# Optimization experiments

Hardware: AMD Instinct MI355X
Metric: run time of the kernel (lower is better)

Reference implementation:

```python
import jax, jax.numpy as jnp
import numpy as np
import math

# ----- sizes -----
NUM_EDGES = 16384
NUM_NODES = 1024          # senders index into [0, NUM_NODES)
N_MUL = 64                # multiplicity n = V.shape[1]
AVG_NEIGH = 16.0          # avg_num_neighbors
F_IN = 64                 # scalar feature dim of x

# ----- real spherical harmonics (component normalization: sum_m Y_lm^2 = 2l+1) -----
_S3 = math.sqrt(3.0); _S5 = math.sqrt(5.0); _S15 = math.sqrt(15.0)
_C33 = math.sqrt(70.0)/4.0; _C32 = math.sqrt(105.0)/2.0
_C31 = math.sqrt(42.0)/4.0; _C30 = math.sqrt(7.0)/2.0; _CXYZ = math.sqrt(105.0)

def _sph(vn):
    x, y, z = vn[:, 0], vn[:, 1], vn[:, 2]
    Y0 = jnp.ones_like(x)[:, None]
    Y1 = _S3 * vn
    Y2 = jnp.stack([_S15*x*y, _S15*y*z, 0.5*_S5*(3*z*z - 1), _S15*x*z, 0.5*_S15*(x*x - y*y)], axis=1)
    Y3 = jnp.stack([_C33*y*(3*x*x - y*y), _CXYZ*x*y*z, _C31*y*(5*z*z - 1), _C30*z*(5*z*z - 3), _C31*x*(5*z*z - 1), _C32*z*(x*x - y*y), _C33*x*(x*x - 3*y*y)], axis=1)
    return [Y0, Y1, Y2, Y3]

# monomial form of the same SH, used to derive EXACT Clebsch-Gordan coefficients
_SHP = {
    0: [[(1.0, (0,0,0))]],
    1: [[(_S3, (1,0,0))], [(_S3, (0,1,0))], [(_S3, (0,0,1))]],
    2: [[(_S15, (1,1,0))], [(_S15, (0,1,1))], [(1.5*_S5, (0,0,2)), (-0.5*_S5, (0,0,0))], [(_S15, (1,0,1))], [(0.5*_S15, (2,0,0)), (-0.5*_S15, (0,2,0))]],
    3: [[(3*_C33, (2,1,0)), (-_C33, (0,3,0))], [(_CXYZ, (1,1,1))], [(5*_C31, (0,1,2)), (-_C31, (0,1,0))], [(5*_C30, (0,0,3)), (-3*_C30, (0,0,1))], [(5*_C31, (1,0,2)), (-_C31, (1,0,0))], [(_C32, (2,0,1)), (-_C32, (0,2,1))], [(_C33, (3,0,0)), (-3*_C33, (1,2,0))]],
}

def _dfact(n):
    r = 1
    while n > 1:
        r *= n; n -= 2
    return r

def _mono_int(e):
    # exact integral of x^a y^b z^c over the unit sphere
    a, b, c = e
    if (a % 2) or (b % 2) or (c % 2):
        return 0.0
    return 4.0*math.pi*_dfact(a-1)*_dfact(b-1)*_dfact(c-1)/_dfact(a+b+c+1)

def _pmul(p, q):
    return [(cp*cq, (a1+a2, b1+b2, c1+c2)) for cp, (a1,b1,c1) in p for cq, (a2,b2,c2) in q]

def _pint(p):
    return sum(c*_mono_int(e) for c, e in p)

def _cg(l1, l2, l3):
    # unique SO(3) intertwiner in this real-SH basis, scaled like e3nn component norm: sqrt(2l3+1)*w3j
    C = np.zeros((2*l1+1, 2*l2+1, 2*l3+1))
    for i, p1 in enumerate(_SHP[l1]):
        for j, p2 in enumerate(_SHP[l2]):
            p12 = _pmul(p1, p2)
            for k, p3 in enumerate(_SHP[l3]):
                C[i, j, k] = _pint(_pmul(p12, p3)) / (4.0*math.pi)
    return jnp.asarray(C / np.linalg.norm(C) * np.sqrt(2*l3+1), dtype=jnp.float32)

# tensor-product paths surviving filter_ir_out = 0e + 1o + 2e (inputs: SH 0e+1o+2e+3o, V 0e+1o+2e)
_PATHS0 = [(0,0), (1,1), (2,2)]
_PATHS1 = [(0,1), (1,0), (1,2), (2,1), (3,2)]
_PATHS2 = [(0,2), (1,1), (2,0), (2,2), (3,1)]
CGS = {(l1, l2, l3): _cg(l1, l2, l3) for l3, ps in ((0, _PATHS0), (1, _PATHS1), (2, _PATHS2)) for l1, l2 in ps}

# e3nn normalize_function(silu): divide by sqrt(E_{z~N(0,1)}[silu(z)^2])
_zg = np.linspace(-12.0, 12.0, 200001)
_phi = np.exp(-0.5*_zg*_zg)/np.sqrt(2.0*np.pi)
_sl = _zg/(1.0 + np.exp(-_zg))
ACT_C = float(np.sqrt(np.sum(_sl*_sl*_phi)*(_zg[1]-_zg[0])))

def _nsilu(v):
    return jax.nn.silu(v) / ACT_C

def _forward(vectors, x, V, senders, W_w, W1, W2, W3, Wv1, Wv2):
    E, n = V.shape[0], V.shape[1]
    d = jnp.linalg.norm(vectors, axis=1, keepdims=True)                 # [E,1] edge lengths
    vn = vectors / d
    Y = jnp.concatenate(_sph(vn), axis=1)                               # [E,16], ell = 0..3
    w = (x @ W_w) / math.sqrt(x.shape[1])                               # [E,n] edge weights (1-layer MLP, no act)
    wY = w[:, :, None] * Y[:, None, :]                                  # [E,n,16]
    agg = jax.ops.segment_sum(wY, senders, num_segments=NUM_NODES)[senders]  # scatter_sum + map_back
    agg = agg / math.sqrt(AVG_NEIGH)
    A = jnp.split(agg, [1, 4, 9], axis=2)                               # SH chunks: dims 1,3,5,7
    B = jnp.split(V, [1, 4], axis=2)                                    # V chunks: dims 1,3,5
    def tp(l1, l2, l3):
        return jnp.einsum('eni,enj,ijk->enk', A[l1], B[l2], CGS[(l1, l2, l3)])
    scal = jnp.concatenate([tp(a, b, 0) for a, b in _PATHS0], axis=2)   # [E,n,3] new scalars
    V1 = jnp.concatenate([tp(a, b, 1) for a, b in _PATHS1], axis=1)     # [E,5n,3] 1o paths
    V2 = jnp.concatenate([tp(a, b, 2) for a, b in _PATHS2], axis=1)     # [E,5n,5] 2e paths
    h = jnp.concatenate([x, scal.reshape(E, 3*n)], axis=1)              # [E, F_IN+3n]
    h = _nsilu(h @ W1 / math.sqrt(h.shape[1]))
    h = _nsilu(h @ W2 / math.sqrt(W2.shape[0]))
    h = h @ W3 / math.sqrt(W3.shape[0])                                 # output_activation=False
    # poly_envelope(p-1=5, 2), p=6: 1 - 28 d^6 + 48 d^7 - 21 d^8 on [0,1), 0 outside
    u = 1.0 - 28.0*d**6 + 48.0*d**7 - 21.0*d**8
    x_out = jnp.where(d < 1.0, u, 0.0) * h                              # [E,64]
    o1 = jnp.einsum('emi,mo->eoi', V1, Wv1) / math.sqrt(V1.shape[1])    # Linear per irrep: [E,n,3]
    o2 = jnp.einsum('emi,mo->eoi', V2, Wv2) / math.sqrt(V2.shape[1])    # [E,n,5]
    # output 0e block has no input path -> zeros (e3nn Linear, no bias)
    V_out = jnp.concatenate([jnp.zeros((E, n, 1), x_out.dtype), o1, o2], axis=2)  # [E,n,9]
    return x_out, V_out

def setup_inputs():
    key = jax.random.key(0)
    ks = jax.random.split(key, 10)
    E = NUM_EDGES
    vectors = 0.35 * jax.random.normal(ks[0], (E, 3), jnp.float32)   # mostly inside cutoff radius 1
    x = jax.random.normal(ks[1], (E, F_IN), jnp.float32)
    V = jax.random.normal(ks[2], (E, N_MUL, 9), jnp.float32)
    senders = jax.random.randint(ks[3], (E,), 0, NUM_NODES, dtype=jnp.int32)
    W_w = jax.random.normal(ks[4], (F_IN, N_MUL), jnp.float32)
    W1 = jax.random.normal(ks[5], (F_IN + 3*N_MUL, 64), jnp.float32)
    W2 = jax.random.normal(ks[6], (64, 64), jnp.float32)
    W3 = jax.random.normal(ks[7], (64, 64), jnp.float32)
    Wv1 = jax.random.normal(ks[8], (5*N_MUL, N_MUL), jnp.float32)
    Wv2 = jax.random.normal(ks[9], (5*N_MUL, N_MUL), jnp.float32)
    return {"vectors": vectors, "x": x, "V": V, "senders": senders, "W_w": W_w, "W1": W1, "W2": W2, "W3": W3, "Wv1": Wv1, "Wv2": Wv2}

def reference(vectors, x, V, senders, W_w, W1, W2, W3, Wv1, Wv2):
    return _forward(vectors, x, V, senders, W_w, W1, W2, W3, Wv1, Wv2)
```

## Files before the change

### kernel.cpp

```cpp
#include <hip/hip_runtime.h>
#include <math.h>

#define NNODES 1024
#define EB 8

typedef __attribute__((ext_vector_type(8))) short short8;
typedef __attribute__((ext_vector_type(4))) float f32x4;

__device__ __forceinline__ unsigned short f2bf(float f) {
  union { float f; unsigned int u; } v; v.f = f;
  unsigned int r = v.u + 0x7fffu + ((v.u >> 16) & 1u);
  return (unsigned short)(r >> 16);
}

struct CGPack { float v[576]; };

static const double H_SHC[16][2] = {
  {1.0, 0.0},
  {1.7320508075688772, 0.0},
  {1.7320508075688772, 0.0},
  {1.7320508075688772, 0.0},
  {3.8729833462074170, 0.0},
  {3.8729833462074170, 0.0},
  {3.3541019662496844, -1.1180339887498949},
  {3.8729833462074170, 0.0},
  {1.9364916731037085, -1.9364916731037085},
  {6.2749501990055667, -2.0916500663351889},
  {10.246950765959598, 0.0},
  {8.1009258730098255, -1.6201851746019651},
  {6.6143782776614768, -3.9686269665968861},
  {8.1009258730098255, -1.6201851746019651},
  {5.1234753829797990, -5.1234753829797990},
  {2.0916500663351889, -6.2749501990055667},
};
static const int H_SHE[16][2] = {
  {0,0},{1,0},{16,0},{256,0},
  {17,0},{272,0},{512,0},{257,0},{2,32},
  {18,48},{273,0},{528,16},{768,256},{513,1},{258,288},{3,33}};
static const int H_PL1[13] = {0,1,2, 0,1,1,2,3, 0,1,2,2,3};
static const int H_PL2[13] = {0,1,2, 1,0,2,1,2, 2,1,0,2,1};
static const int H_PL3[13] = {0,0,0, 1,1,1,1,1, 2,2,2,2,2};
static const int H_PCG[13] = {0,1,10, 35,44,53,98,143, 248,273,318,343,468};

static double h_dfact(int n) { double r = 1.0; while (n > 1) { r *= n; n -= 2; } return r; }

struct HostConsts {
  CGPack pack;
  float inv_actc;
  HostConsts() {
    const int LOFF[4] = {0,1,4,9};
    for (int p = 0; p < 13; p++) {
      int l1 = H_PL1[p], l2 = H_PL2[p], l3 = H_PL3[p];
      int n1 = 2*l1+1, n2 = 2*l2+1, n3 = 2*l3+1, nent = n1*n2*n3;
      double vals[125], ss = 0.0;
      for (int t = 0; t < nent; t++) {
        int i = t / (n2*n3);
        int rem = t - i*(n2*n3);
        int j = rem / n3;
        int k = rem - j*n3;
        int lm1 = LOFF[l1]+i, lm2 = LOFF[l2]+j, lm3 = LOFF[l3]+k;
        double v = 0.0;
        for (int t1 = 0; t1 < 2; t1++)
        for (int t2 = 0; t2 < 2; t2++)
        for (int t3 = 0; t3 < 2; t3++) {
          double cc = H_SHC[lm1][t1]*H_SHC[lm2][t2]*H_SHC[lm3][t3];
          if (cc == 0.0) continue;
          int s = H_SHE[lm1][t1] + H_SHE[lm2][t2] + H_SHE[lm3][t3];
          int a = s & 15, b = (s >> 4) & 15, c = (s >> 8) & 15;
          if (!((a|b|c) & 1))
            v += cc * (h_dfact(a-1)*h_dfact(b-1)*h_dfact(c-1) / h_dfact(a+b+c+1));
        }
        vals[t] = v; ss += v*v;
      }
      double scale = sqrt((double)(2*l3+1)) / sqrt(ss);
      for (int t = 0; t < nent; t++) pack.v[H_PCG[p]+t] = (float)(vals[t]*scale*0.25);
    }
    pack.v[573] = pack.v[574] = pack.v[575] = 0.f;
    double s = 0.0, dz = 24.0/200000.0;
    for (int i = 0; i <= 200000; i++) {
      double z = -12.0 + dz*i;
      double ph = exp(-0.5*z*z) * 0.39894228040143267794;
      double sl = z / (1.0 + exp(-z));
      s += sl*sl*ph;
    }
    inv_actc = (float)(1.0 / sqrt(s*dz));
  }
};

__global__ __launch_bounds__(256) void k_pre(
    const int* __restrict__ senders, int* __restrict__ counts, int* __restrict__ elist,
    const float* __restrict__ Wv1, const float* __restrict__ Wv2,
    const float* __restrict__ W1, const float* __restrict__ W2, const float* __restrict__ W3,
    unsigned short* __restrict__ wv1f, unsigned short* __restrict__ wv2f,
    unsigned short* __restrict__ w1f, unsigned short* __restrict__ w2f,
    unsigned short* __restrict__ w3f,
    float inv_actc, int E)
{
  const int t = threadIdx.x;
  const int nsc = gridDim.x - 32;
  if ((int)blockIdx.x < nsc) {
    int e = blockIdx.x*256 + t;
    if (e < E) {
      int s = senders[e];
      int pos = atomicAdd(&counts[s], 1) & 63;
      elist[s*64 + pos] = e;
    }
    return;
  }
  const int wid = t >> 6, lane = t & 63;
  const int g = (blockIdx.x - nsc)*4 + wid;
  const float ia = inv_actc;
  const float s320 = 0.05590169943749474f;
  const float* src; unsigned short* dst; int nk, f; float sc;
  if (g < 40)       { src = Wv1; dst = wv1f; nk = 10; f = g;       sc = s320; }
  else if (g < 80)  { src = Wv2; dst = wv2f; nk = 10; f = g - 40;  sc = s320; }
  else if (g < 112) { src = W1;  dst = w1f;  nk = 8;  f = g - 80;  sc = 0.0625f; }
  else if (g < 120) { src = W2;  dst = w2f;  nk = 2;  f = g - 112; sc = 0.125f*ia; }
  else              { src = W3;  dst = w3f;  nk = 2;  f = g - 120; sc = 0.125f*ia; }
  int nt = f / nk;
  int ks = f - nt*nk;
  unsigned short us[8];
  #pragma unroll
  for (int j = 0; j < 8; j++) {
    float v = src[(ks*32 + (lane>>4)*8 + j)*64 + nt*16 + (lane & 15)];
    us[j] = f2bf(v * sc);
  }
  uint4 pk;
  pk.x = (unsigned)us[0] | ((unsigned)us[1] << 16);
  pk.y = (unsigned)us[2] | ((unsigned)us[3] << 16);
  pk.z = (unsigned)us[4] | ((unsigned)us[5] << 16);
  pk.w = (unsigned)us[6] | ((unsigned)us[7] << 16);
  *(uint4*)(dst + ((size_t)f*64 + lane)*8) = pk;
}

__global__ __launch_bounds__(256, 2) void k_node(
    const float* __restrict__ vec, const float* __restrict__ x,
    const float* __restrict__ Ww,
    const int* __restrict__ counts, const int* __restrict__ elist,
    float* __restrict__ node_agg)
{
  __shared__ float red[4*1024];
  const int wid = threadIdx.x >> 6, lane = threadIdx.x & 63;
  const int s = blockIdx.x;
  const int deg = min(counts[s], 64);

  float ww[64];
  #pragma unroll
  for (int f = 0; f < 64; f++) ww[f] = Ww[f*64 + lane];

  const float S3 = 1.7320508075688772f, S5 = 2.23606797749979f, S15 = 3.872983346207417f;
  const float C33 = 2.091650066335189f, C32 = 5.123475382979799f, C31 = 1.6201851746019651f;
  const float C30 = 1.3228756555322954f, CX = 10.246950765959598f;

  float A[16];
  #pragma unroll
  for (int k = 0; k < 16; k++) A[k] = 0.f;

  for (int ii = wid; ii < deg; ii += 4) {
    int e = elist[s*64 + ii];
    float xv = x[(size_t)e*64 + lane];
    float w0 = 0.f, w1 = 0.f, w2 = 0.f, w3 = 0.f;
    #pragma unroll
    for (int f = 0; f < 64; f += 4) {
      w0 = fmaf(__shfl(xv, f+0), ww[f+0], w0);
      w1 = fmaf(__shfl(xv, f+1), ww[f+1], w1);
      w2 = fmaf(__shfl(xv, f+2), ww[f+2], w2);
      w3 = fmaf(__shfl(xv, f+3), ww[f+3], w3);
    }
    float w = ((w0+w1)+(w2+w3)) * 0.125f;
    float vx = vec[e*3+0], vy = vec[e*3+1], vz = vec[e*3+2];
    float d = sqrtf(vx*vx + vy*vy + vz*vz);
    float X = vx/d, Yv = vy/d, Z = vz/d;
    float y[16];
    y[0] = 1.f;
    y[1] = S3*X;  y[2] = S3*Yv;  y[3] = S3*Z;
    y[4] = S15*X*Yv; y[5] = S15*Yv*Z; y[6] = 0.5f*S5*(3.f*Z*Z - 1.f);
    y[7] = S15*X*Z;  y[8] = 0.5f*S15*(X*X - Yv*Yv);
    y[9]  = C33*Yv*(3.f*X*X - Yv*Yv);
    y[10] = CX*X*Yv*Z;
    y[11] = C31*Yv*(5.f*Z*Z - 1.f);
    y[12] = C30*Z*(5.f*Z*Z - 3.f);
    y[13] = C31*X*(5.f*Z*Z - 1.f);
    y[14] = C32*Z*(X*X - Yv*Yv);
    y[15] = C33*X*(X*X - 3.f*Yv*Yv);
    #pragma unroll
    for (int k = 0; k < 16; k++) A[k] = fmaf(w, y[k], A[k]);
  }
  #pragma unroll
  for (int k = 0; k < 16; k++) red[wid*1024 + lane*16 + k] = A[k];
  __syncthreads();
  const int t = threadIdx.x;
  f32x4 v0 = ((f32x4*)red)[t];
  f32x4 v1 = ((f32x4*)red)[256 + t];
  f32x4 v2 = ((f32x4*)red)[512 + t];
  f32x4 v3 = ((f32x4*)red)[768 + t];
  f32x4 sum = v0 + v1 + v2 + v3;
  ((f32x4*)(node_agg + (size_t)s*1024))[t] = sum;
}

template<int L1, int L2, int L3>
__device__ __forceinline__ void tp_path(const float* __restrict__ cgp,
    const float a[16], const float b[9], float o[2*L3+1])
{
  constexpr int N1 = 2*L1+1, N2 = 2*L2+1, N3 = 2*L3+1;
  constexpr int AO = (L1==0) ? 0 : (L1==1) ? 1 : (L1==2) ? 4 : 9;
  constexpr int BO = (L2==0) ? 0 : (L2==1) ? 1 : 4;
  constexpr int LM1 = (L1==0) ? 0 : (L1==1) ? 1 : (L1==2) ? 4 : 9;
  constexpr int LM2 = (L2==0) ? 0 : (L2==1) ? 1 : 4;
  constexpr int LM3 = (L3==0) ? 0 : (L3==1) ? 1 : 4;
  static constexpr unsigned char PAR[16] =
      {0, 1,2,4, 3,6,0,5,0, 2,7,2,4,1,4,1};
  #pragma unroll
  for (int k = 0; k < N3; k++) o[k] = 0.f;
  int ci = 0;
  #pragma unroll
  for (int i = 0; i < N1; i++) {
    #pragma unroll
    for (int j = 0; j < N2; j++) {
      float ab = a[AO+i] * b[BO+j];
      #pragma unroll
      for (int k = 0; k < N3; k++) {
        if ((PAR[LM1+i] ^ PAR[LM2+j] ^ PAR[LM3+k]) == 0)
          o[k] = fmaf(ab, cgp[ci], o[k]);
        ci++;
      }
    }
  }
}

__global__ __launch_bounds__(256, 3) void edge_main(
    const float* __restrict__ vec, const float* __restrict__ x,
    const float* __restrict__ V, const int* __restrict__ senders,
    const float* __restrict__ node_agg, const CGPack P,
    const unsigned short* __restrict__ wv1f, const unsigned short* __restrict__ wv2f,
    const unsigned short* __restrict__ w1f, const unsigned short* __restrict__ w2f,
    const unsigned short* __restrict__ w3f,
    float* __restrict__ out, int E)
{
  __shared__ __align__(16) unsigned short V12sh[64*328];
  __shared__ __align__(16) unsigned short zrow[336];
  __shared__ __align__(16) unsigned short hsh[8*264];
  __shared__ __align__(16) unsigned short h1sh[8*72];
  __shared__ __align__(16) unsigned short h2sh[8*72];
  __shared__ __align__(16) float xosh[8*64];
  __shared__ float ush[EB];

  unsigned short* V1sh = V12sh;
  unsigned short* V2sh = V12sh + 24*328;
  float* vosh = (float*)V12sh;

  const float* cg = P.v;

  const int t = threadIdx.x;
  const int wid = t >> 6, lane = t & 63;
  const int e0 = blockIdx.x * EB;
  const size_t E64 = (size_t)E * 64;

  if (t < 168) ((unsigned int*)zrow)[t] = 0u;

  if (t < 128) {
    int el = t >> 4, off = (t & 15)*4;
    f32x4 xv = *(const f32x4*)(x + (size_t)(e0 + el)*64 + off);
    uint2 pk;
    pk.x = (unsigned)f2bf(xv.x) | ((unsigned)f2bf(xv.y) << 16);
    pk.y = (unsigned)f2bf(xv.z) | ((unsigned)f2bf(xv.w) << 16);
    *(uint2*)(hsh + el*264 + off) = pk;
  }

  #pragma unroll
  for (int sub = 0; sub < 2; sub++) {
    const int eloc = wid*2 + sub;
    const int eg = e0 + eloc;

    float b[9];
    const float* vp = V + (size_t)eg*576 + lane*9;
    #pragma unroll
    for (int j = 0; j < 9; j++) b[j] = vp[j];

    const int s = senders[eg];
    float a[16];
    const float* nap = node_agg + s*1024 + lane*16;
    #pragma unroll
    for (int k = 0; k < 16; k++) a[k] = nap[k];

    float o1[1], o3[3], o5[5];
    tp_path<0,0,0>(cg + 0,  a, b, o1); hsh[eloc*264 + 64 + lane*3 + 0] = f2bf(o1[0]);
    tp_path<1,1,0>(cg + 1,  a, b, o1); hsh[eloc*264 + 64 + lane*3 + 1] = f2bf(o1[0]);
    tp_path<2,2,0>(cg + 10, a, b, o1); hsh[eloc*264 + 64 + lane*3 + 2] = f2bf(o1[0]);
    tp_path<0,1,1>(cg + 35, a, b, o3);
    { int r = eloc*3; for (int i=0;i<3;i++) V1sh[(r+i)*328 + 0*64 + lane] = f2bf(o3[i]); }
    tp_path<1,0,1>(cg + 44, a, b, o3);
    { int r = eloc*3; for (int i=0;i<3;i++) V1sh[(r+i)*328 + 1*64 + lane] = f2bf(o3[i]); }
    tp_path<1,2,1>(cg + 53, a, b, o3);
    { int r = eloc*3; for (int i=0;i<3;i++) V1sh[(r+i)*328 + 2*64 + lane] = f2bf(o3[i]); }
    tp_path<2,1,1>(cg + 98, a, b, o3);
    { int r = eloc*3; for (int i=0;i<3;i++) V1sh[(r+i)*328 + 3*64 + lane] = f2bf(o3[i]); }
    tp_path<3,2,1>(cg + 143, a, b, o3);
    { int r = eloc*3; for (int i=0;i<3;i++) V1sh[(r+i)*328 + 4*64 + lane] = f2bf(o3[i]); }
    tp_path<0,2,2>(cg + 248, a, b, o5);
    { int r = eloc*5; for (int i=0;i<5;i++) V2sh[(r+i)*328 + 0*64 + lane] = f2bf(o5[i]); }
    tp_path<1,1,2>(cg + 273, a, b, o5);
    { int r = eloc*5; for (int i=0;i<5;i++) V2sh[(r+i)*328 + 1*64 + lane] = f2bf(o5[i]); }
    tp_path<2,0,2>(cg + 318, a, b, o5);
    { int r = eloc*5; for (int i=0;i<5;i++) V2sh[(r+i)*328 + 2*64 + lane] = f2bf(o5[i]); }
    tp_path<2,2,2>(cg + 343, a, b, o5);
    { int r = eloc*5; for (int i=0;i<5;i++) V2sh[(r+i)*328 + 3*64 + lane] = f2bf(o5[i]); }
    tp_path<3,1,2>(cg + 468, a, b, o5);
    { int r = eloc*5; for (int i=0;i<5;i++) V2sh[(r+i)*328 + 4*64 + lane] = f2bf(o5[i]); }

    if (lane == 0) {
      float vx = vec[eg*3+0], vy = vec[eg*3+1], vz = vec[eg*3+2];
      float d = sqrtf(vx*vx + vy*vy + vz*vz);
      float u = 0.f;
      if (d < 1.f) {
        float d3 = d*d*d, d6 = d3*d3, d7 = d6*d, d8 = d7*d;
        u = 1.f - 28.f*d6 + 48.f*d7 - 21.f*d8;
      }
      ush[eloc] = u;
    }
  }
  __syncthreads();

  const int ntile = wid;
  const int qr = lane >> 4;
  const int ml = lane & 15;

  f32x4 acc1a = (f32x4){0,0,0,0}, acc1b = (f32x4){0,0,0,0};
  {
    const unsigned short* p0 = &V1sh[ml*328];
    const unsigned short* p1 = (16+ml < 24) ? &V1sh[(16+ml)*328] : zrow;
    const unsigned short* bb = wv1f + ((size_t)(ntile*10)*64 + lane)*8;
    #pragma unroll
    for (int ks = 0; ks < 10; ks++) {
      short8 bf = *(const short8*)(bb + ks*512);
      int ao = ks*32 + qr*8;
      short8 af0 = *(const short8*)(p0 + ao);
      short8 af1 = *(const short8*)(p1 + ao);
      acc1a = __builtin_amdgcn_mfma_f32_16x16x32_bf16(af0, bf, acc1a, 0, 0, 0);
      acc1b = __builtin_amdgcn_mfma_f32_16x16x32_bf16(af1, bf, acc1b, 0, 0, 0);
    }
  }

  f32x4 acc2a = (f32x4){0,0,0,0}, acc2b = (f32x4){0,0,0,0}, acc2c = (f32x4){0,0,0,0};
  {
    const unsigned short* p0 = &V2sh[ml*328];
    const unsigned short* p1 = &V2sh[(16+ml)*328];
    const unsigned short* p2 = (32+ml < 40) ? &V2sh[(32+ml)*328] : zrow;
    const unsigned short* bb = wv2f + ((size_t)(ntile*10)*64 + lane)*8;
    #pragma unroll
    for (int ks = 0; ks < 10; ks++) {
      short8 bf = *(const short8*)(bb + ks*512);
      int ao = ks*32 + qr*8;
      short8 af0 = *(const short8*)(p0 + ao);
      short8 af1 = *(const short8*)(p1 + ao);
      short8 af2 = *(const short8*)(p2 + ao);
      acc2a = __builtin_amdgcn_mfma_f32_16x16x32_bf16(af0, bf, acc2a, 0, 0, 0);
      acc2b = __builtin_amdgcn_mfma_f32_16x16x32_bf16(af1, bf, acc2b, 0, 0, 0);
      acc2c = __builtin_amdgcn_mfma_f32_16x16x32_bf16(af2, bf, acc2c, 0, 0, 0);
    }
  }

  {
    f32x4 c = (f32x4){0,0,0,0};
    const unsigned short* hp = (ml < 8) ? &hsh[ml*264] : zrow;
    const unsigned short* bb = w1f + ((size_t)(ntile*8)*64 + lane)*8;
    #pragma unroll
    for (int ks = 0; ks < 8; ks++) {
      short8 bf = *(const short8*)(bb + ks*512);
      short8 af = *(const short8*)(hp + ks*32 + qr*8);
      c = __builtin_amdgcn_mfma_f32_16x16x32_bf16(af, bf, c, 0, 0, 0);
    }
    #pragma unroll
    for (int r = 0; r < 4; r++) {
      int row = qr*4 + r;
      if (row < 8) {
        float v = c[r];
        float sv = v / (1.f + expf(-v));
        h1sh[row*72 + ntile*16 + ml] = f2bf(sv);
      }
    }
  }
  __syncthreads();

  #pragma unroll
  for (int r = 0; r < 4; r++) {
    int row = qr*4 + r;
    int el = row / 3, i = row - (row/3)*3;
    vosh[el*584 + (ntile*16+ml)*9 + 1 + i] = acc1a[r];
  }
  #pragma unroll
  for (int r = 0; r < 4; r++) {
    int row = 16 + qr*4 + r;
    if (row < 24) {
      int el = row / 3, i = row - (row/3)*3;
      vosh[el*584 + (ntile*16+ml)*9 + 1 + i] = acc1b[r];
    }
  }
  #pragma unroll
  for (int r = 0; r < 4; r++) {
    int row = qr*4 + r;
    int el = row / 5, i = row - (row/5)*5;
    vosh[el*584 + (ntile*16+ml)*9 + 4 + i] = acc2a[r];
  }
  #pragma unroll
  for (int r = 0; r < 4; r++) {
    int row = 16 + qr*4 + r;
    int el = row / 5, i = row - (row/5)*5;
    vosh[el*584 + (ntile*16+ml)*9 + 4 + i] = acc2b[r];
  }
  #pragma unroll
  for (int r = 0; r < 4; r++) {
    int row = 32 + qr*4 + r;
    if (row < 40) {
      int el = row / 5, i = row - (row/5)*5;
      vosh[el*584 + (ntile*16+ml)*9 + 4 + i] = acc2c[r];
    }
  }
  for (int q = t; q < 8*64; q += 256) {
    int el = q >> 6, n = q & 63;
    vosh[el*584 + n*9] = 0.f;
  }

  {
    f32x4 c = (f32x4){0,0,0,0};
    const unsigned short* ap = (ml < 8) ? &h1sh[ml*72] : zrow;
    const unsigned short* bb = w2f + ((size_t)(ntile*2)*64 + lane)*8;
    #pragma unroll
    for (int ks = 0; ks < 2; ks++) {
      short8 bf = *(const short8*)(bb + ks*512);
      short8 af = *(const short8*)(ap + ks*32 + qr*8);
      c = __builtin_amdgcn_mfma_f32_16x16x32_bf16(af, bf, c, 0, 0, 0);
    }
    #pragma unroll
    for (int r = 0; r < 4; r++) {
      int row = qr*4 + r;
      if (row < 8) {
        float v = c[r];
        float sv = v / (1.f + expf(-v));
        h2sh[row*72 + ntile*16 + ml] = f2bf(sv);
      }
    }
  }
  __syncthreads();

  {
    f32x4 c = (f32x4){0,0,0,0};
    const unsigned short* ap = (ml < 8) ? &h2sh[ml*72] : zrow;
    const unsigned short* bb = w3f + ((size_t)(ntile*2)*64 + lane)*8;
    #pragma unroll
    for (int ks = 0; ks < 2; ks++) {
      short8 bf = *(const short8*)(bb + ks*512);
      short8 af = *(const short8*)(ap + ks*32 + qr*8);
      c = __builtin_amdgcn_mfma_f32_16x16x32_bf16(af, bf, c, 0, 0, 0);
    }
    #pragma unroll
    for (int r = 0; r < 4; r++) {
      int row = qr*4 + r;
      if (row < 8) xosh[row*64 + ntile*16 + ml] = ush[row] * c[r];
    }
  }

  for (int q = t; q < 8*144; q += 256) {
    int el = q / 144, i4 = q - (q/144)*144;
    ((f32x4*)(out + E64 + (size_t)(e0+el)*576))[i4] = ((f32x4*)(vosh + el*584))[i4];
  }
  __syncthreads();

  if (t < 128)
    ((f32x4*)(out + (size_t)e0*64))[t] = ((f32x4*)xosh)[t];
}

extern "C" void kernel_launch(void* const* d_in, const int* in_sizes, int n_in,
                              void* d_out, int out_size, void* d_ws, size_t ws_size,
                              hipStream_t stream)
{
  const float* vec     = (const float*)d_in[0];
  const float* x       = (const float*)d_in[1];
  const float* V       = (const float*)d_in[2];
  const int*   senders = (const int*)  d_in[3];
  const float* Ww      = (const float*)d_in[4];
  const float* W1      = (const float*)d_in[5];
  const float* W2      = (const float*)d_in[6];
  const float* W3      = (const float*)d_in[7];
  const float* Wv1     = (const float*)d_in[8];
  const float* Wv2     = (const float*)d_in[9];
  float* out = (float*)d_out;
  const int E = in_sizes[0] / 3;

  static HostConsts HC;

  char* base = (char*)d_ws;
  float* node_agg = (float*)(base);
  int* counts     = (int*)  (base + (8<<20) + 8192);
  int* elist      = (int*)  (base + (8<<20) + 12288);
  unsigned short* wv1f = (unsigned short*)(base + (8<<20) + 278528);
  unsigned short* wv2f = (unsigned short*)(base + (8<<20) + 319488);
  unsigned short* w1f  = (unsigned short*)(base + (8<<20) + 360448);
  unsigned short* w2f  = (unsigned short*)(base + (8<<20) + 393216);
  unsigned short* w3f  = (unsigned short*)(base + (8<<20) + 401408);

  hipMemsetAsync(counts, 0, NNODES*sizeof(int), stream);

  const int nsc = (E + 255) >> 8;
  k_pre<<<nsc + 32, 256, 0, stream>>>(senders, counts, elist,
                                      Wv1, Wv2, W1, W2, W3,
                                      wv1f, wv2f, w1f, w2f, w3f, HC.inv_actc, E);
  k_node<<<NNODES, 256, 0, stream>>>(vec, x, Ww, counts, elist, node_agg);
  edge_main<<<E/EB, 256, 0, stream>>>(vec, x, V, senders, node_agg, HC.pack,
                                      wv1f, wv2f, w1f, w2f, w3f, out, E);
}
```

Before: 171.8 us.

## Precompute edge weights in k_pre and halve edges per block in edge_main

Moves the per-edge x·W_w product out of k_node's gather loop into extra k_pre blocks that tile 64 edges in shared memory and write the result to a workspace buffer. k_node then only loads the precomputed weight instead of running a shuffle-based matvec for every neighbour. edge_main now handles 4 edges per block, one per wave, instead of 8. Its shared-memory footprint shrinks and the launch bound rises to 6 blocks per CU to raise occupancy, at the cost of more padded MFMA rows and twice as many blocks. A redundant dead y[14] assignment is also added.

New measurement: 165.9 us. 1.04x faster.

```diff
diff --git a/kernel.cpp b/kernel.cpp
--- a/kernel.cpp
+++ b/kernel.cpp
@@ -2,7 +2,7 @@
 #include <math.h>
 
 #define NNODES 1024
-#define EB 8
+#define EB 4
 
 typedef __attribute__((ext_vector_type(8))) short short8;
 typedef __attribute__((ext_vector_type(4))) float f32x4;
@@ -89,6 +89,8 @@
 
 __global__ __launch_bounds__(256) void k_pre(
     const int* __restrict__ senders, int* __restrict__ counts, int* __restrict__ elist,
+    const float* __restrict__ x, const float* __restrict__ Ww,
+    float* __restrict__ w_ws,
     const float* __restrict__ Wv1, const float* __restrict__ Wv2,
     const float* __restrict__ W1, const float* __restrict__ W2, const float* __restrict__ W3,
     unsigned short* __restrict__ wv1f, unsigned short* __restrict__ wv2f,
@@ -97,9 +99,11 @@
     float inv_actc, int E)
 {
   const int t = threadIdx.x;
-  const int nsc = gridDim.x - 32;
-  if ((int)blockIdx.x < nsc) {
-    int e = blockIdx.x*256 + t;
+  const int bid = blockIdx.x;
+  const int nsc = (E + 255) >> 8;
+
+  if (bid < nsc) {
+    int e = bid*256 + t;
     if (e < E) {
       int s = senders[e];
       int pos = atomicAdd(&counts[s], 1) & 63;
@@ -107,35 +111,66 @@
     }
     return;
   }
-  const int wid = t >> 6, lane = t & 63;
-  const int g = (blockIdx.x - nsc)*4 + wid;
-  const float ia = inv_actc;
-  const float s320 = 0.05590169943749474f;
-  const float* src; unsigned short* dst; int nk, f; float sc;
-  if (g < 40)       { src = Wv1; dst = wv1f; nk = 10; f = g;       sc = s320; }
-  else if (g < 80)  { src = Wv2; dst = wv2f; nk = 10; f = g - 40;  sc = s320; }
-  else if (g < 112) { src = W1;  dst = w1f;  nk = 8;  f = g - 80;  sc = 0.0625f; }
-  else if (g < 120) { src = W2;  dst = w2f;  nk = 2;  f = g - 112; sc = 0.125f*ia; }
-  else              { src = W3;  dst = w3f;  nk = 2;  f = g - 120; sc = 0.125f*ia; }
-  int nt = f / nk;
-  int ks = f - nt*nk;
-  unsigned short us[8];
-  #pragma unroll
-  for (int j = 0; j < 8; j++) {
-    float v = src[(ks*32 + (lane>>4)*8 + j)*64 + nt*16 + (lane & 15)];
-    us[j] = f2bf(v * sc);
-  }
-  uint4 pk;
-  pk.x = (unsigned)us[0] | ((unsigned)us[1] << 16);
-  pk.y = (unsigned)us[2] | ((unsigned)us[3] << 16);
-  pk.z = (unsigned)us[4] | ((unsigned)us[5] << 16);
-  pk.w = (unsigned)us[6] | ((unsigned)us[7] << 16);
-  *(uint4*)(dst + ((size_t)f*64 + lane)*8) = pk;
+
+  if (bid < nsc + 32) {
+    const int wid = t >> 6, lane = t & 63;
+    const int g = (bid - nsc)*4 + wid;
+    const float ia = inv_actc;
+    const float s320 = 0.05590169943749474f;
+    const float* src; unsigned short* dst; int nk, f; float sc;
+    if (g < 40)       { src = Wv1; dst = wv1f; nk = 10; f = g;       sc = s320; }
+    else if (g < 80)  { src = Wv2; dst = wv2f; nk = 10; f = g - 40;  sc = s320; }
+    else if (g < 112) { src = W1;  dst = w1f;  nk = 8;  f = g - 80;  sc = 0.0625f; }
+    else if (g < 120) { src = W2;  dst = w2f;  nk = 2;  f = g - 112; sc = 0.125f*ia; }
+    else              { src = W3;  dst = w3f;  nk = 2;  f = g - 120; sc = 0.125f*ia; }
+    int nt = f / nk;
+    int ks = f - nt*nk;
+    unsigned short us[8];
+    #pragma unroll
+    for (int j = 0; j < 8; j++) {
+      float v = src[(ks*32 + (lane>>4)*8 + j)*64 + nt*16 + (lane & 15)];
+      us[j] = f2bf(v * sc);
+    }
+    uint4 pk;
+    pk.x = (unsigned)us[0] | ((unsigned)us[1] << 16);
+    pk.y = (unsigned)us[2] | ((unsigned)us[3] << 16);
+    pk.z = (unsigned)us[4] | ((unsigned)us[5] << 16);
+    pk.w = (unsigned)us[6] | ((unsigned)us[7] << 16);
+    *(uint4*)(dst + ((size_t)f*64 + lane)*8) = pk;
+    return;
+  }
+
+  __shared__ float xsh[64*64];
+  const int eb0 = (bid - nsc - 32) * 64;
+  for (int q = t; q < 1024; q += 256)
+    ((f32x4*)xsh)[q] = ((const f32x4*)(x + (size_t)eb0*64))[q];
+
+  const int n = t & 63;
+  float ww[64];
+  #pragma unroll
+  for (int f = 0; f < 64; f++) ww[f] = Ww[f*64 + n];
+  __syncthreads();
+
+  const int er0 = (t >> 6) * 16;
+  #pragma unroll
+  for (int i = 0; i < 16; i++) {
+    int e = er0 + i;
+    const f32x4* xr = (const f32x4*)(&xsh[e*64]);
+    float a0 = 0.f, a1 = 0.f, a2 = 0.f, a3 = 0.f;
+    #pragma unroll
+    for (int fq = 0; fq < 16; fq += 4) {
+      f32x4 x0 = xr[fq+0], x1 = xr[fq+1], x2 = xr[fq+2], x3 = xr[fq+3];
+      a0 = fmaf(x0.x, ww[fq*4+0],  fmaf(x0.y, ww[fq*4+1],  fmaf(x0.z, ww[fq*4+2],  fmaf(x0.w, ww[fq*4+3],  a0))));
+      a1 = fmaf(x1.x, ww[fq*4+4],  fmaf(x1.y, ww[fq*4+5],  fmaf(x1.z, ww[fq*4+6],  fmaf(x1.w, ww[fq*4+7],  a1))));
+      a2 = fmaf(x2.x, ww[fq*4+8],  fmaf(x2.y, ww[fq*4+9],  fmaf(x2.z, ww[fq*4+10], fmaf(x2.w, ww[fq*4+11], a2))));
+      a3 = fmaf(x3.x, ww[fq*4+12], fmaf(x3.y, ww[fq*4+13], fmaf(x3.z, ww[fq*4+14], fmaf(x3.w, ww[fq*4+15], a3))));
+    }
+    w_ws[(size_t)(eb0+e)*64 + n] = ((a0+a1)+(a2+a3)) * 0.125f;
+  }
 }
 
-__global__ __launch_bounds__(256, 2) void k_node(
-    const float* __restrict__ vec, const float* __restrict__ x,
-    const float* __restrict__ Ww,
+__global__ __launch_bounds__(256) void k_node(
+    const float* __restrict__ vec, const float* __restrict__ w_ws,
     const int* __restrict__ counts, const int* __restrict__ elist,
     float* __restrict__ node_agg)
 {
@@ -144,10 +179,6 @@
   const int s = blockIdx.x;
   const int deg = min(counts[s], 64);
 
-  float ww[64];
-  #pragma unroll
-  for (int f = 0; f < 64; f++) ww[f] = Ww[f*64 + lane];
-
   const float S3 = 1.7320508075688772f, S5 = 2.23606797749979f, S15 = 3.872983346207417f;
   const float C33 = 2.091650066335189f, C32 = 5.123475382979799f, C31 = 1.6201851746019651f;
   const float C30 = 1.3228756555322954f, CX = 10.246950765959598f;
@@ -158,16 +189,7 @@
 
   for (int ii = wid; ii < deg; ii += 4) {
     int e = elist[s*64 + ii];
-    float xv = x[(size_t)e*64 + lane];
-    float w0 = 0.f, w1 = 0.f, w2 = 0.f, w3 = 0.f;
-    #pragma unroll
-    for (int f = 0; f < 64; f += 4) {
-      w0 = fmaf(__shfl(xv, f+0), ww[f+0], w0);
-      w1 = fmaf(__shfl(xv, f+1), ww[f+1], w1);
-      w2 = fmaf(__shfl(xv, f+2), ww[f+2], w2);
-      w3 = fmaf(__shfl(xv, f+3), ww[f+3], w3);
-    }
-    float w = ((w0+w1)+(w2+w3)) * 0.125f;
+    float wv = w_ws[(size_t)e*64 + lane];
     float vx = vec[e*3+0], vy = vec[e*3+1], vz = vec[e*3+2];
     float d = sqrtf(vx*vx + vy*vy + vz*vz);
     float X = vx/d, Yv = vy/d, Z = vz/d;
@@ -181,10 +203,11 @@
     y[11] = C31*Yv*(5.f*Z*Z - 1.f);
     y[12] = C30*Z*(5.f*Z*Z - 3.f);
     y[13] = C31*X*(5.f*Z*Z - 1.f);
+    y[14] = C32*Z*(X*X - 3.f*Yv*Yv)*0.f + C32*Z*(X*X - Yv*Yv);
     y[14] = C32*Z*(X*X - Yv*Yv);
     y[15] = C33*X*(X*X - 3.f*Yv*Yv);
     #pragma unroll
-    for (int k = 0; k < 16; k++) A[k] = fmaf(w, y[k], A[k]);
+    for (int k = 0; k < 16; k++) A[k] = fmaf(wv, y[k], A[k]);
   }
   #pragma unroll
   for (int k = 0; k < 16; k++) red[wid*1024 + lane*16 + k] = A[k];
@@ -228,7 +251,7 @@
   }
 }
 
-__global__ __launch_bounds__(256, 3) void edge_main(
+__global__ __launch_bounds__(256, 6) void edge_main(
     const float* __restrict__ vec, const float* __restrict__ x,
     const float* __restrict__ V, const int* __restrict__ senders,
     const float* __restrict__ node_agg, const CGPack P,
@@ -237,16 +260,16 @@
     const unsigned short* __restrict__ w3f,
     float* __restrict__ out, int E)
 {
-  __shared__ __align__(16) unsigned short V12sh[64*328];
+  __shared__ __align__(16) unsigned short V12sh[32*328];
   __shared__ __align__(16) unsigned short zrow[336];
-  __shared__ __align__(16) unsigned short hsh[8*264];
-  __shared__ __align__(16) unsigned short h1sh[8*72];
-  __shared__ __align__(16) unsigned short h2sh[8*72];
-  __shared__ __align__(16) float xosh[8*64];
+  __shared__ __align__(16) unsigned short hsh[4*264];
+  __shared__ __align__(16) unsigned short h1sh[4*72];
+  __shared__ __align__(16) unsigned short h2sh[4*72];
+  __shared__ __align__(16) float xosh[4*64];
   __shared__ float ush[EB];
 
   unsigned short* V1sh = V12sh;
-  unsigned short* V2sh = V12sh + 24*328;
+  unsigned short* V2sh = V12sh + 12*328;
   float* vosh = (float*)V12sh;
 
   const float* cg = P.v;
@@ -258,7 +281,7 @@
 
   if (t < 168) ((unsigned int*)zrow)[t] = 0u;
 
-  if (t < 128) {
+  if (t < 64) {
     int el = t >> 4, off = (t & 15)*4;
     f32x4 xv = *(const f32x4*)(x + (size_t)(e0 + el)*64 + off);
     uint2 pk;
@@ -267,9 +290,8 @@
     *(uint2*)(hsh + el*264 + off) = pk;
   }
 
-  #pragma unroll
-  for (int sub = 0; sub < 2; sub++) {
-    const int eloc = wid*2 + sub;
+  {
+    const int eloc = wid;
     const int eg = e0 + eloc;
 
     float b[9];
@@ -279,9 +301,12 @@
 
     const int s = senders[eg];
     float a[16];
-    const float* nap = node_agg + s*1024 + lane*16;
-    #pragma unroll
-    for (int k = 0; k < 16; k++) a[k] = nap[k];
+    const f32x4* nap = (const f32x4*)(node_agg + s*1024 + lane*16);
+    #pragma unroll
+    for (int q = 0; q < 4; q++) {
+      f32x4 av = nap[q];
+      a[q*4+0] = av.x; a[q*4+1] = av.y; a[q*4+2] = av.z; a[q*4+3] = av.w;
+    }
 
     float o1[1], o3[3], o5[5];
     tp_path<0,0,0>(cg + 0,  a, b, o1); hsh[eloc*264 + 64 + lane*3 + 0] = f2bf(o1[0]);
@@ -325,44 +350,37 @@
   const int qr = lane >> 4;
   const int ml = lane & 15;
 
-  f32x4 acc1a = (f32x4){0,0,0,0}, acc1b = (f32x4){0,0,0,0};
+  f32x4 acc1 = (f32x4){0,0,0,0};
   {
-    const unsigned short* p0 = &V1sh[ml*328];
-    const unsigned short* p1 = (16+ml < 24) ? &V1sh[(16+ml)*328] : zrow;
+    const unsigned short* p0 = (ml < 12) ? &V1sh[ml*328] : zrow;
     const unsigned short* bb = wv1f + ((size_t)(ntile*10)*64 + lane)*8;
+    #pragma unroll
+    for (int ks = 0; ks < 10; ks++) {
+      short8 bf = *(const short8*)(bb + ks*512);
+      short8 af = *(const short8*)(p0 + ks*32 + qr*8);
+      acc1 = __builtin_amdgcn_mfma_f32_16x16x32_bf16(af, bf, acc1, 0, 0, 0);
+    }
+  }
+
+  f32x4 acc2a = (f32x4){0,0,0,0}, acc2b = (f32x4){0,0,0,0};
+  {
+    const unsigned short* p0 = &V2sh[ml*328];
+    const unsigned short* p1 = (16+ml < 20) ? &V2sh[(16+ml)*328] : zrow;
+    const unsigned short* bb = wv2f + ((size_t)(ntile*10)*64 + lane)*8;
     #pragma unroll
     for (int ks = 0; ks < 10; ks++) {
       short8 bf = *(const short8*)(bb + ks*512);
       int ao = ks*32 + qr*8;
       short8 af0 = *(const short8*)(p0 + ao);
       short8 af1 = *(const short8*)(p1 + ao);
-      acc1a = __builtin_amdgcn_mfma_f32_16x16x32_bf16(af0, bf, acc1a, 0, 0, 0);
-      acc1b = __builtin_amdgcn_mfma_f32_16x16x32_bf16(af1, bf, acc1b, 0, 0, 0);
-    }
-  }
-
-  f32x4 acc2a = (f32x4){0,0,0,0}, acc2b = (f32x4){0,0,0,0}, acc2c = (f32x4){0,0,0,0};
-  {
-    const unsigned short* p0 = &V2sh[ml*328];
-    const unsigned short* p1 = &V2sh[(16+ml)*328];
-    const unsigned short* p2 = (32+ml < 40) ? &V2sh[(32+ml)*328] : zrow;
-    const unsigned short* bb = wv2f + ((size_t)(ntile*10)*64 + lane)*8;
-    #pragma unroll
-    for (int ks = 0; ks < 10; ks++) {
-      short8 bf = *(const short8*)(bb + ks*512);
-      int ao = ks*32 + qr*8;
-      short8 af0 = *(const short8*)(p0 + ao);
-      short8 af1 = *(const short8*)(p1 + ao);
-      short8 af2 = *(const short8*)(p2 + ao);
       acc2a = __builtin_amdgcn_mfma_f32_16x16x32_bf16(af0, bf, acc2a, 0, 0, 0);
       acc2b = __builtin_amdgcn_mfma_f32_16x16x32_bf16(af1, bf, acc2b, 0, 0, 0);
-      acc2c = __builtin_amdgcn_mfma_f32_16x16x32_bf16(af2, bf, acc2c, 0, 0, 0);
-    }
-  }
-
+    }
+  }
+
+  const unsigned short* hp = (ml < 4) ? &hsh[ml*264] : zrow;
   {
     f32x4 c = (f32x4){0,0,0,0};
-    const unsigned short* hp = (ml < 8) ? &hsh[ml*264] : zrow;
     const unsigned short* bb = w1f + ((size_t)(ntile*8)*64 + lane)*8;
     #pragma unroll
     for (int ks = 0; ks < 8; ks++) {
@@ -373,7 +391,7 @@
     #pragma unroll
     for (int r = 0; r < 4; r++) {
       int row = qr*4 + r;
-      if (row < 8) {
+      if (row < 4) {
         float v = c[r];
         float sv = v / (1.f + expf(-v));
         h1sh[row*72 + ntile*16 + ml] = f2bf(sv);
@@ -385,15 +403,9 @@
   #pragma unroll
   for (int r = 0; r < 4; r++) {
     int row = qr*4 + r;
-    int el = row / 3, i = row - (row/3)*3;
-    vosh[el*584 + (ntile*16+ml)*9 + 1 + i] = acc1a[r];
-  }
-  #pragma unroll
-  for (int r = 0; r < 4; r++) {
-    int row = 16 + qr*4 + r;
-    if (row < 24) {
+    if (row < 12) {
       int el = row / 3, i = row - (row/3)*3;
-      vosh[el*584 + (ntile*16+ml)*9 + 1 + i] = acc1b[r];
+      vosh[el*584 + (ntile*16+ml)*9 + 1 + i] = acc1[r];
     }
   }
   #pragma unroll
@@ -405,25 +417,17 @@
   #pragma unroll
   for (int r = 0; r < 4; r++) {
     int row = 16 + qr*4 + r;
-    int el = row / 5, i = row - (row/5)*5;
-    vosh[el*584 + (ntile*16+ml)*9 + 4 + i] = acc2b[r];
-  }
-  #pragma unroll
-  for (int r = 0; r < 4; r++) {
-    int row = 32 + qr*4 + r;
-    if (row < 40) {
+    if (row < 20) {
       int el = row / 5, i = row - (row/5)*5;
-      vosh[el*584 + (ntile*16+ml)*9 + 4 + i] = acc2c[r];
-    }
-  }
-  for (int q = t; q < 8*64; q += 256) {
-    int el = q >> 6, n = q & 63;
-    vosh[el*584 + n*9] = 0.f;
-  }
+      vosh[el*584 + (ntile*16+ml)*9 + 4 + i] = acc2b[r];
+    }
+  }
+  { int el = t >> 6, o = t & 63;
+    vosh[el*584 + o*9] = 0.f; }
 
   {
     f32x4 c = (f32x4){0,0,0,0};
-    const unsigned short* ap = (ml < 8) ? &h1sh[ml*72] : zrow;
+    const unsigned short* ap = (ml < 4) ? &h1sh[ml*72] : zrow;
     const unsigned short* bb = w2f + ((size_t)(ntile*2)*64 + lane)*8;
     #pragma unroll
     for (int ks = 0; ks < 2; ks++) {
@@ -434,7 +438,7 @@
     #pragma unroll
     for (int r = 0; r < 4; r++) {
       int row = qr*4 + r;
-      if (row < 8) {
+      if (row < 4) {
         float v = c[r];
         float sv = v / (1.f + expf(-v));
         h2sh[row*72 + ntile*16 + ml] = f2bf(sv);
@@ -445,7 +449,7 @@
 
   {
     f32x4 c = (f32x4){0,0,0,0};
-    const unsigned short* ap = (ml < 8) ? &h2sh[ml*72] : zrow;
+    const unsigned short* ap = (ml < 4) ? &h2sh[ml*72] : zrow;
     const unsigned short* bb = w3f + ((size_t)(ntile*2)*64 + lane)*8;
     #pragma unroll
     for (int ks = 0; ks < 2; ks++) {
@@ -456,17 +460,17 @@
     #pragma unroll
     for (int r = 0; r < 4; r++) {
       int row = qr*4 + r;
-      if (row < 8) xosh[row*64 + ntile*16 + ml] = ush[row] * c[r];
-    }
-  }
-
-  for (int q = t; q < 8*144; q += 256) {
+      if (row < 4) xosh[row*64 + ntile*16 + ml] = ush[row] * c[r];
+    }
+  }
+
+  for (int q = t; q < 576; q += 256) {
     int el = q / 144, i4 = q - (q/144)*144;
     ((f32x4*)(out + E64 + (size_t)(e0+el)*576))[i4] = ((f32x4*)(vosh + el*584))[i4];
   }
   __syncthreads();
 
-  if (t < 128)
+  if (t < 64)
     ((f32x4*)(out + (size_t)e0*64))[t] = ((f32x4*)xosh)[t];
 }
 
@@ -491,6 +495,7 @@
 
   char* base = (char*)d_ws;
   float* node_agg = (float*)(base);
+  float* w_ws     = (float*)(base + (4<<20));
   int* counts     = (int*)  (base + (8<<20) + 8192);
   int* elist      = (int*)  (base + (8<<20) + 12288);
   unsigned short* wv1f = (unsigned short*)(base + (8<<20) + 278528);
@@ -502,10 +507,12 @@
   hipMemsetAsync(counts, 0, NNODES*sizeof(int), stream);
 
   const int nsc = (E + 255) >> 8;
-  k_pre<<<nsc + 32, 256, 0, stream>>>(senders, counts, elist,
+  const int ngemm = (E + 63) >> 6;
+  k_pre<<<nsc + 32 + ngemm, 256, 0, stream>>>(senders, counts, elist,
+                                      x, Ww, w_ws,
                                       Wv1, Wv2, W1, W2, W3,
                                       wv1f, wv2f, w1f, w2f, w3f, HC.inv_actc, E);
-  k_node<<<NNODES, 256, 0, stream>>>(vec, x, Ww, counts, elist, node_agg);
+  k_node<<<NNODES, 256, 0, stream>>>(vec, w_ws, counts, elist, node_agg);
   edge_main<<<E/EB, 256, 0, stream>>>(vec, x, V, senders, node_agg, HC.pack,
                                       wv1f, wv2f, w1f, w2f, w3f, out, E);
 }
```
